# Kernel optimization log

Measured on AMD Instinct MI355X. Metric: run time of the kernel, lower is better.

The kernel has to match this reference:

```python
import jax, jax.numpy as jnp
import numpy as np

E = 768
H = 12
D = E // H  # 64


def setup_inputs() -> dict:
    key = jax.random.key(0)
    ks = jax.random.split(key, 12)
    B, S = 4, 2048
    scale = 1.0 / np.sqrt(E)
    inp = {
        "q": jax.random.normal(ks[0], (B, S, E), jnp.float32),
        "k": jax.random.normal(ks[1], (B, S, E), jnp.float32),
        "v": jax.random.normal(ks[2], (B, S, E), jnp.float32),
        "mask": jax.random.randint(ks[3], (B, S), 0, 2, jnp.int32),
        "Wq": jax.random.normal(ks[4], (E, E), jnp.float32) * scale,
        "bq": jnp.zeros((E,), jnp.float32),
        "Wk": jax.random.normal(ks[5], (E, E), jnp.float32) * scale,
        "bk": jnp.zeros((E,), jnp.float32),
        "Wv": jax.random.normal(ks[6], (E, E), jnp.float32) * scale,
        "bv": jnp.zeros((E,), jnp.float32),
        "Wo": jax.random.normal(ks[7], (E, E), jnp.float32) * scale,
        "bo": jnp.zeros((E,), jnp.float32),
    }
    return inp


def reference(q, k, v, mask, Wq, bq, Wk, bk, Wv, bv, Wo, bo):
    B, Sq, _ = q.shape
    Sk = k.shape[1]
    # QKV projections, split into heads: [B, H, S, D]
    qh = (q @ Wq + bq).reshape(B, Sq, H, D).transpose(0, 2, 1, 3)
    kh = (k @ Wk + bk).reshape(B, Sk, H, D).transpose(0, 2, 1, 3)
    vh = (v @ Wv + bv).reshape(B, Sk, H, D).transpose(0, 2, 1, 3)
    scores = jnp.einsum("bhqd,bhkd->bhqk", qh, kh) / jnp.sqrt(jnp.float32(D))
    # enc=True padding-mask path: positions where mask==0 get -1e9 added
    bias = jnp.where(mask == 0, jnp.float32(-1e9), jnp.float32(0.0))  # [B, Sk]
    scores = scores + bias[:, None, None, :]
    weights = jax.nn.softmax(scores, axis=-1)
    # dropout is identity in eval mode
    ctx = jnp.einsum("bhqk,bhkd->bqhd", weights, vh).reshape(B, Sq, E)
    return ctx @ Wo + bo
```

## Files before the change

kernel.cpp:

```cpp
#include <hip/hip_runtime.h>
#include <hip/hip_bf16.h>
#include <stdint.h>


typedef __bf16 bf16x8 __attribute__((ext_vector_type(8)));
typedef __bf16 bf16x4 __attribute__((ext_vector_type(4)));
typedef float floatx4 __attribute__((ext_vector_type(4)));

#define MFMA_BF16(a, b, c) __builtin_amdgcn_mfma_f32_16x16x32_bf16(a, b, c, 0, 0, 0)


__device__ __forceinline__ void glds16(const __bf16* g, __bf16* l) {
  __builtin_amdgcn_global_load_lds(
      (const __attribute__((address_space(1))) unsigned int*)g,
      (__attribute__((address_space(3))) unsigned int*)l, 16, 0, 0);
}

__global__ __launch_bounds__(256) void prep_transpose(
    const float* __restrict__ W0, const float* __restrict__ W1,
    const float* __restrict__ W2, const float* __restrict__ W3,
    __bf16* __restrict__ T0, __bf16* __restrict__ T1,
    __bf16* __restrict__ T2, __bf16* __restrict__ T3) {
  const int z = blockIdx.z;
  const float* W = (z == 0) ? W0 : (z == 1) ? W1 : (z == 2) ? W2 : W3;
  __bf16* T = (z == 0) ? T0 : (z == 1) ? T1 : (z == 2) ? T2 : T3;
  __shared__ float t[32][33];
  const int tx = threadIdx.x & 31, ty = threadIdx.x >> 5;
  const int kb = blockIdx.x * 32, nb = blockIdx.y * 32;
#pragma unroll
  for (int j = 0; j < 4; ++j)
    t[ty + j * 8][tx] = W[(size_t)(kb + ty + j * 8) * 768 + nb + tx];
  __syncthreads();
#pragma unroll
  for (int j = 0; j < 4; ++j)
    T[(size_t)(nb + ty + j * 8) * 768 + kb + tx] = (__bf16)t[tx][ty + j * 8];
}

__global__ __launch_bounds__(256) void qkv_gemm(
    const __bf16* __restrict__ Wtq, const __bf16* __restrict__ Wtk,
    const __bf16* __restrict__ Wtv, const float* __restrict__ Xq,
    const float* __restrict__ Xk, const float* __restrict__ Xv,
    const float* __restrict__ bq, const float* __restrict__ bk,
    const float* __restrict__ bv, __bf16* __restrict__ Qh,
    __bf16* __restrict__ Kh, __bf16* __restrict__ Vt) {
  __shared__ __align__(16) __bf16 As[128 * 32];
  __shared__ __align__(16) __bf16 Bs[128 * 32];
  const int z = blockIdx.z;
  const __bf16* Aop = (z == 0) ? Wtq : (z == 1) ? Wtk : Wtv;
  const float* Bop = (z == 0) ? Xq : (z == 1) ? Xk : Xv;
  const float* bias = (z == 0) ? bq : (z == 1) ? bk : bv;
  __bf16* Dst = (z == 0) ? Qh : (z == 1) ? Kh : Vt;
  const int m0 = blockIdx.x * 128, n0 = blockIdx.y * 128;

  const int tid = threadIdx.x, lane = tid & 63, w = tid >> 6;
  const int quad = lane >> 4, l16 = lane & 15;
  const int wm = (w >> 1) * 64, wn = (w & 1) * 64;

  const int garow = w * 32 + (lane >> 2);
  const int gacol = (lane & 3) * 8;
  const __bf16* gA = Aop + (size_t)(m0 + garow) * 768 + gacol;
  __bf16* lA = As + w * 1024;
  const int brow = tid >> 3, bcol = (tid & 7) * 4;

  floatx4 acc[4][4] = {};

  for (int k0 = 0; k0 < 768; k0 += 32) {
    __syncthreads();
    glds16(gA, lA);
    glds16(gA + (size_t)16 * 768, lA + 512);
    gA += 32;
    float4 f[4];
#pragma unroll
    for (int j = 0; j < 4; ++j)
      f[j] = *(const float4*)&Bop[(size_t)(n0 + brow + 32 * j) * 768 + k0 + bcol];
#pragma unroll
    for (int j = 0; j < 4; ++j) {
      bf16x4 pv;
      pv[0] = (__bf16)f[j].x; pv[1] = (__bf16)f[j].y;
      pv[2] = (__bf16)f[j].z; pv[3] = (__bf16)f[j].w;
      *(bf16x4*)&Bs[(brow + 32 * j) * 32 + bcol] = pv;
    }
    __syncthreads();
    bf16x8 af[4], bfr[4];
#pragma unroll
    for (int t = 0; t < 4; ++t) {
      af[t] = *(const bf16x8*)&As[(wm + t * 16 + l16) * 32 + quad * 8];
      bfr[t] = *(const bf16x8*)&Bs[(wn + t * 16 + l16) * 32 + quad * 8];
    }
#pragma unroll
    for (int mt = 0; mt < 4; ++mt)
#pragma unroll
      for (int nt = 0; nt < 4; ++nt)
        acc[mt][nt] = MFMA_BF16(af[mt], bfr[nt], acc[mt][nt]);
  }

#pragma unroll
  for (int mt = 0; mt < 4; ++mt) {
    const int e = m0 + wm + mt * 16 + quad * 4;
    const float4 b4 = *(const float4*)&bias[e];
    const int h = e >> 6, d = e & 63;
#pragma unroll
    for (int nt = 0; nt < 4; ++nt) {
      const int s = n0 + wn + nt * 16 + l16;
      const int bb = s >> 11, sr = s & 2047;
      const float v0 = acc[mt][nt][0] + b4.x;
      const float v1 = acc[mt][nt][1] + b4.y;
      const float v2 = acc[mt][nt][2] + b4.z;
      const float v3 = acc[mt][nt][3] + b4.w;
      if (z < 2) {
        bf16x4 pv;
        pv[0] = (__bf16)v0; pv[1] = (__bf16)v1; pv[2] = (__bf16)v2; pv[3] = (__bf16)v3;
        *(bf16x4*)&Dst[((size_t)(bb * 12 + h) * 2048 + sr) * 64 + d] = pv;
      } else {
        const size_t base = ((size_t)(bb * 12 + h) * 64 + d) * 2048 + sr;
        Dst[base] = (__bf16)v0;
        Dst[base + 2048] = (__bf16)v1;
        Dst[base + 4096] = (__bf16)v2;
        Dst[base + 6144] = (__bf16)v3;
      }
    }
  }
}

__global__ __launch_bounds__(256) void out_gemm(const __bf16* __restrict__ Wto,
                                                const __bf16* __restrict__ Ctx,
                                                const float* __restrict__ bo,
                                                float* __restrict__ Out) {
  __shared__ __align__(16) __bf16 As[128 * 32];
  __shared__ __align__(16) __bf16 Bs[128 * 32];
  const int m0 = blockIdx.x * 128, n0 = blockIdx.y * 128;
  const int tid = threadIdx.x, lane = tid & 63, w = tid >> 6;
  const int quad = lane >> 4, l16 = lane & 15;
  const int wm = (w >> 1) * 64, wn = (w & 1) * 64;

  const int grow = w * 32 + (lane >> 2);
  const int gcol = (lane & 3) * 8;
  const __bf16* gA = Wto + (size_t)(m0 + grow) * 768 + gcol;
  const __bf16* gB = Ctx + (size_t)(n0 + grow) * 768 + gcol;
  __bf16* lA = As + w * 1024;
  __bf16* lB = Bs + w * 1024;

  floatx4 acc[4][4] = {};
  for (int k0 = 0; k0 < 768; k0 += 32) {
    __syncthreads();
    glds16(gA, lA);
    glds16(gA + (size_t)16 * 768, lA + 512);
    glds16(gB, lB);
    glds16(gB + (size_t)16 * 768, lB + 512);
    gA += 32;
    gB += 32;
    __syncthreads();
    bf16x8 af[4], bfr[4];
#pragma unroll
    for (int t = 0; t < 4; ++t) {
      af[t] = *(const bf16x8*)&As[(wm + t * 16 + l16) * 32 + quad * 8];
      bfr[t] = *(const bf16x8*)&Bs[(wn + t * 16 + l16) * 32 + quad * 8];
    }
#pragma unroll
    for (int mt = 0; mt < 4; ++mt)
#pragma unroll
      for (int nt = 0; nt < 4; ++nt)
        acc[mt][nt] = MFMA_BF16(af[mt], bfr[nt], acc[mt][nt]);
  }

#pragma unroll
  for (int mt = 0; mt < 4; ++mt) {
    const int e = m0 + wm + mt * 16 + quad * 4;
    const float4 b4 = *(const float4*)&bo[e];
#pragma unroll
    for (int nt = 0; nt < 4; ++nt) {
      const int s = n0 + wn + nt * 16 + l16;
      float4 r;
      r.x = acc[mt][nt][0] + b4.x;
      r.y = acc[mt][nt][1] + b4.y;
      r.z = acc[mt][nt][2] + b4.z;
      r.w = acc[mt][nt][3] + b4.w;
      *(float4*)&Out[(size_t)s * 768 + e] = r;
    }
  }
}

__global__ __launch_bounds__(256) void attn_kernel(
    const __bf16* __restrict__ Qh, const __bf16* __restrict__ Kh,
    const __bf16* __restrict__ Vt, const int* __restrict__ mask,
    __bf16* __restrict__ ctx) {
  const int bh = blockIdx.y, b = bh / 12, h = bh - b * 12;
  const int tid = threadIdx.x, lane = tid & 63, w = tid >> 6;
  const int quad = lane >> 4, l16 = lane & 15;
  const int q0 = blockIdx.x * 128 + w * 32;

  __shared__ float biasS[2048];
  __shared__ __align__(16) __bf16 Ks[64 * 64];
  __shared__ __align__(16) __bf16 Vs[64 * 64];
  __shared__ __align__(16) __bf16 Plds[4][32][72];

  for (int i = tid; i < 2048; i += 256)
    biasS[i] = mask[b * 2048 + i] ? 0.0f : -1e5f;
  __syncthreads();

  const __bf16* Qbase = Qh + (size_t)bh * 2048 * 64;
  const __bf16* Kbase = Kh + (size_t)bh * 2048 * 64;
  const __bf16* Vbase = Vt + (size_t)bh * 64 * 2048;

  bf16x8 bqf[2][2];
#pragma unroll
  for (int qt = 0; qt < 2; ++qt)
#pragma unroll
    for (int c = 0; c < 2; ++c)
      bqf[qt][c] =
          *(const bf16x8*)&Qbase[(size_t)(q0 + qt * 16 + l16) * 64 + c * 32 + quad * 8];

  const int srow = (lane >> 3);
  const int scol = (lane & 7) * 8;

  floatx4 o[4][2] = {};
  float rS[2] = {0.0f, 0.0f};
  const float SC = 0.18033688011112042f;

  for (int kt = 0; kt < 2048; kt += 64) {
    __syncthreads();
#pragma unroll
    for (int j = 0; j < 2; ++j) {
      const int c = w * 2 + j;
      const int row = c * 8 + srow;
      glds16(&Kbase[(size_t)(kt + row) * 64 + scol], Ks + c * 512);
      glds16(&Vbase[(size_t)row * 2048 + kt + scol], Vs + c * 512);
    }
    __syncthreads();

    floatx4 sc[4][2];
#pragma unroll
    for (int t = 0; t < 4; ++t) {
      bf16x8 ak0 = *(const bf16x8*)&Ks[(t * 16 + l16) * 64 + quad * 8];
      bf16x8 ak1 = *(const bf16x8*)&Ks[(t * 16 + l16) * 64 + 32 + quad * 8];
#pragma unroll
      for (int qt = 0; qt < 2; ++qt) {
        floatx4 zz = {};
        zz = MFMA_BF16(ak0, bqf[qt][0], zz);
        zz = MFMA_BF16(ak1, bqf[qt][1], zz);
        sc[t][qt] = zz;
      }
    }
#pragma unroll
    for (int t = 0; t < 4; ++t) {
      const float4 kb = *(const float4*)&biasS[kt + t * 16 + quad * 4];
#pragma unroll
      for (int qt = 0; qt < 2; ++qt) {
        floatx4 p;
        p[0] = exp2f(fmaf(sc[t][qt][0], SC, kb.x));
        p[1] = exp2f(fmaf(sc[t][qt][1], SC, kb.y));
        p[2] = exp2f(fmaf(sc[t][qt][2], SC, kb.z));
        p[3] = exp2f(fmaf(sc[t][qt][3], SC, kb.w));
        sc[t][qt] = p;
        rS[qt] += p[0] + p[1] + p[2] + p[3];
      }
    }
#pragma unroll
    for (int qt = 0; qt < 2; ++qt)
#pragma unroll
      for (int t = 0; t < 4; ++t) {
        bf16x4 pv;
        pv[0] = (__bf16)sc[t][qt][0];
        pv[1] = (__bf16)sc[t][qt][1];
        pv[2] = (__bf16)sc[t][qt][2];
        pv[3] = (__bf16)sc[t][qt][3];
        *(bf16x4*)&Plds[w][qt * 16 + l16][t * 16 + quad * 4] = pv;
      }
#pragma unroll
    for (int c = 0; c < 2; ++c) {
      bf16x8 bp[2];
#pragma unroll
      for (int qt = 0; qt < 2; ++qt)
        bp[qt] = *(const bf16x8*)&Plds[w][qt * 16 + l16][c * 32 + quad * 8];
#pragma unroll
      for (int dt = 0; dt < 4; ++dt) {
        bf16x8 av = *(const bf16x8*)&Vs[(dt * 16 + l16) * 64 + c * 32 + quad * 8];
#pragma unroll
        for (int qt = 0; qt < 2; ++qt) o[dt][qt] = MFMA_BF16(av, bp[qt], o[dt][qt]);
      }
    }
  }

  float inv[2];
#pragma unroll
  for (int qt = 0; qt < 2; ++qt) {
    float s = rS[qt];
    s += __shfl_xor(s, 16, 64);
    s += __shfl_xor(s, 32, 64);
    inv[qt] = 1.0f / s;
  }
#pragma unroll
  for (int dt = 0; dt < 4; ++dt)
#pragma unroll
    for (int qt = 0; qt < 2; ++qt) {
      const int q = q0 + qt * 16 + l16;
      const int d = h * 64 + dt * 16 + quad * 4;
      bf16x4 pv;
      pv[0] = (__bf16)(o[dt][qt][0] * inv[qt]);
      pv[1] = (__bf16)(o[dt][qt][1] * inv[qt]);
      pv[2] = (__bf16)(o[dt][qt][2] * inv[qt]);
      pv[3] = (__bf16)(o[dt][qt][3] * inv[qt]);
      *(bf16x4*)&ctx[(size_t)(b * 2048 + q) * 768 + d] = pv;
    }
}

extern "C" void kernel_launch(void* const* d_in, const int* in_sizes, int n_in,
                              void* d_out, int out_size, void* d_ws, size_t ws_size,
                              hipStream_t stream) {
  const float* q = (const float*)d_in[0];
  const float* k = (const float*)d_in[1];
  const float* v = (const float*)d_in[2];
  const int* mask = (const int*)d_in[3];
  const float* Wq = (const float*)d_in[4];
  const float* bq = (const float*)d_in[5];
  const float* Wk = (const float*)d_in[6];
  const float* bk = (const float*)d_in[7];
  const float* Wv = (const float*)d_in[8];
  const float* bv = (const float*)d_in[9];
  const float* Wo = (const float*)d_in[10];
  const float* bo = (const float*)d_in[11];
  float* out = (float*)d_out;

  char* ws = (char*)d_ws;
  const size_t SZ = (size_t)8192 * 768 * 2;
  const size_t WSZ = (size_t)768 * 768 * 2;
  __bf16* Qh = (__bf16*)(ws);
  __bf16* Kh = (__bf16*)(ws + SZ);
  __bf16* Vt = (__bf16*)(ws + 2 * SZ);
  __bf16* ctx = (__bf16*)(ws + 3 * SZ);
  __bf16* Wtq = (__bf16*)(ws + 4 * SZ);
  __bf16* Wtk = (__bf16*)(ws + 4 * SZ + WSZ);
  __bf16* Wtv = (__bf16*)(ws + 4 * SZ + 2 * WSZ);
  __bf16* Wto = (__bf16*)(ws + 4 * SZ + 3 * WSZ);

  prep_transpose<<<dim3(24, 24, 4), 256, 0, stream>>>(Wq, Wk, Wv, Wo, Wtq, Wtk, Wtv, Wto);
  qkv_gemm<<<dim3(6, 64, 3), 256, 0, stream>>>(Wtq, Wtk, Wtv, q, k, v, bq, bk, bv,
                                               Qh, Kh, Vt);
  attn_kernel<<<dim3(16, 48), 256, 0, stream>>>(Qh, Kh, Vt, mask, ctx);
  out_gemm<<<dim3(6, 64), 256, 0, stream>>>(Wto, ctx, bo, out);
}
```

Baseline: 333.9 us.

## Pre-convert activations to bf16 and XOR-swizzle K/V layouts to avoid LDS conflicts

New measurement: 320.2 us. 4.1% less time.

```diff
diff --git a/kernel.cpp b/kernel.cpp
--- a/kernel.cpp
+++ b/kernel.cpp
@@ -14,6 +14,22 @@
   __builtin_amdgcn_global_load_lds(
       (const __attribute__((address_space(1))) unsigned int*)g,
       (__attribute__((address_space(3))) unsigned int*)l, 16, 0, 0);
+}
+
+__global__ __launch_bounds__(256) void prep_convert(
+    const float* __restrict__ q, const float* __restrict__ k,
+    const float* __restrict__ v, __bf16* __restrict__ Xq,
+    __bf16* __restrict__ Xk, __bf16* __restrict__ Xv) {
+  const int z = blockIdx.y;
+  const float* src = (z == 0) ? q : (z == 1) ? k : v;
+  __bf16* dst = (z == 0) ? Xq : (z == 1) ? Xk : Xv;
+  const size_t i8 = ((size_t)blockIdx.x * 256 + threadIdx.x) * 8;
+  float4 f0 = *(const float4*)&src[i8];
+  float4 f1 = *(const float4*)&src[i8 + 4];
+  bf16x8 o;
+  o[0] = (__bf16)f0.x; o[1] = (__bf16)f0.y; o[2] = (__bf16)f0.z; o[3] = (__bf16)f0.w;
+  o[4] = (__bf16)f1.x; o[5] = (__bf16)f1.y; o[6] = (__bf16)f1.z; o[7] = (__bf16)f1.w;
+  *(bf16x8*)&dst[i8] = o;
 }
 
 __global__ __launch_bounds__(256) void prep_transpose(
@@ -38,8 +54,8 @@
 
 __global__ __launch_bounds__(256) void qkv_gemm(
     const __bf16* __restrict__ Wtq, const __bf16* __restrict__ Wtk,
-    const __bf16* __restrict__ Wtv, const float* __restrict__ Xq,
-    const float* __restrict__ Xk, const float* __restrict__ Xv,
+    const __bf16* __restrict__ Wtv, const __bf16* __restrict__ Xq,
+    const __bf16* __restrict__ Xk, const __bf16* __restrict__ Xv,
     const float* __restrict__ bq, const float* __restrict__ bk,
     const float* __restrict__ bv, __bf16* __restrict__ Qh,
     __bf16* __restrict__ Kh, __bf16* __restrict__ Vt) {
@@ -47,7 +63,7 @@
   __shared__ __align__(16) __bf16 Bs[128 * 32];
   const int z = blockIdx.z;
   const __bf16* Aop = (z == 0) ? Wtq : (z == 1) ? Wtk : Wtv;
-  const float* Bop = (z == 0) ? Xq : (z == 1) ? Xk : Xv;
+  const __bf16* Bop = (z == 0) ? Xq : (z == 1) ? Xk : Xv;
   const float* bias = (z == 0) ? bq : (z == 1) ? bk : bv;
   __bf16* Dst = (z == 0) ? Qh : (z == 1) ? Kh : Vt;
   const int m0 = blockIdx.x * 128, n0 = blockIdx.y * 128;
@@ -56,11 +72,12 @@
   const int quad = lane >> 4, l16 = lane & 15;
   const int wm = (w >> 1) * 64, wn = (w & 1) * 64;
 
-  const int garow = w * 32 + (lane >> 2);
-  const int gacol = (lane & 3) * 8;
-  const __bf16* gA = Aop + (size_t)(m0 + garow) * 768 + gacol;
+  const int grow = w * 32 + (lane >> 2);
+  const int gcol = (lane & 3) * 8;
+  const __bf16* gA = Aop + (size_t)(m0 + grow) * 768 + gcol;
+  const __bf16* gB = Bop + (size_t)(n0 + grow) * 768 + gcol;
   __bf16* lA = As + w * 1024;
-  const int brow = tid >> 3, bcol = (tid & 7) * 4;
+  __bf16* lB = Bs + w * 1024;
 
   floatx4 acc[4][4] = {};
 
@@ -68,18 +85,10 @@
     __syncthreads();
     glds16(gA, lA);
     glds16(gA + (size_t)16 * 768, lA + 512);
+    glds16(gB, lB);
+    glds16(gB + (size_t)16 * 768, lB + 512);
     gA += 32;
-    float4 f[4];
-#pragma unroll
-    for (int j = 0; j < 4; ++j)
-      f[j] = *(const float4*)&Bop[(size_t)(n0 + brow + 32 * j) * 768 + k0 + bcol];
-#pragma unroll
-    for (int j = 0; j < 4; ++j) {
-      bf16x4 pv;
-      pv[0] = (__bf16)f[j].x; pv[1] = (__bf16)f[j].y;
-      pv[2] = (__bf16)f[j].z; pv[3] = (__bf16)f[j].w;
-      *(bf16x4*)&Bs[(brow + 32 * j) * 32 + bcol] = pv;
-    }
+    gB += 32;
     __syncthreads();
     bf16x8 af[4], bfr[4];
 #pragma unroll
@@ -110,13 +119,15 @@
       if (z < 2) {
         bf16x4 pv;
         pv[0] = (__bf16)v0; pv[1] = (__bf16)v1; pv[2] = (__bf16)v2; pv[3] = (__bf16)v3;
-        *(bf16x4*)&Dst[((size_t)(bb * 12 + h) * 2048 + sr) * 64 + d] = pv;
+        const int col = (z == 0) ? d : ((((d >> 3) ^ (sr & 7)) << 3) | (d & 7));
+        *(bf16x4*)&Dst[((size_t)(bb * 12 + h) * 2048 + sr) * 64 + col] = pv;
       } else {
-        const size_t base = ((size_t)(bb * 12 + h) * 64 + d) * 2048 + sr;
-        Dst[base] = (__bf16)v0;
-        Dst[base + 2048] = (__bf16)v1;
-        Dst[base + 4096] = (__bf16)v2;
-        Dst[base + 6144] = (__bf16)v3;
+        const size_t rowbase = ((size_t)(bb * 12 + h) * 64 + d) * 2048;
+        const int shi = sr & ~63, sblk = (sr >> 3) & 7, soff = sr & 7;
+        Dst[rowbase + 0 * 2048 + shi + (((sblk ^ ((d + 0) & 7))) << 3) + soff] = (__bf16)v0;
+        Dst[rowbase + 1 * 2048 + shi + (((sblk ^ ((d + 1) & 7))) << 3) + soff] = (__bf16)v1;
+        Dst[rowbase + 2 * 2048 + shi + (((sblk ^ ((d + 2) & 7))) << 3) + soff] = (__bf16)v2;
+        Dst[rowbase + 3 * 2048 + shi + (((sblk ^ ((d + 3) & 7))) << 3) + soff] = (__bf16)v3;
       }
     }
   }
@@ -212,6 +223,7 @@
 
   const int srow = (lane >> 3);
   const int scol = (lane & 7) * 8;
+  const int col0 = (quad ^ (l16 & 7)) * 8;
 
   floatx4 o[4][2] = {};
   float rS[2] = {0.0f, 0.0f};
@@ -231,8 +243,8 @@
     floatx4 sc[4][2];
 #pragma unroll
     for (int t = 0; t < 4; ++t) {
-      bf16x8 ak0 = *(const bf16x8*)&Ks[(t * 16 + l16) * 64 + quad * 8];
-      bf16x8 ak1 = *(const bf16x8*)&Ks[(t * 16 + l16) * 64 + 32 + quad * 8];
+      bf16x8 ak0 = *(const bf16x8*)&Ks[(t * 16 + l16) * 64 + col0];
+      bf16x8 ak1 = *(const bf16x8*)&Ks[(t * 16 + l16) * 64 + (col0 ^ 32)];
 #pragma unroll
       for (int qt = 0; qt < 2; ++qt) {
         floatx4 zz = {};
@@ -274,7 +286,7 @@
         bp[qt] = *(const bf16x8*)&Plds[w][qt * 16 + l16][c * 32 + quad * 8];
 #pragma unroll
       for (int dt = 0; dt < 4; ++dt) {
-        bf16x8 av = *(const bf16x8*)&Vs[(dt * 16 + l16) * 64 + c * 32 + quad * 8];
+        bf16x8 av = *(const bf16x8*)&Vs[(dt * 16 + l16) * 64 + (col0 ^ (c * 32))];
 #pragma unroll
         for (int qt = 0; qt < 2; ++qt) o[dt][qt] = MFMA_BF16(av, bp[qt], o[dt][qt]);
       }
@@ -324,17 +336,21 @@
   char* ws = (char*)d_ws;
   const size_t SZ = (size_t)8192 * 768 * 2;
   const size_t WSZ = (size_t)768 * 768 * 2;
-  __bf16* Qh = (__bf16*)(ws);
-  __bf16* Kh = (__bf16*)(ws + SZ);
-  __bf16* Vt = (__bf16*)(ws + 2 * SZ);
-  __bf16* ctx = (__bf16*)(ws + 3 * SZ);
-  __bf16* Wtq = (__bf16*)(ws + 4 * SZ);
-  __bf16* Wtk = (__bf16*)(ws + 4 * SZ + WSZ);
-  __bf16* Wtv = (__bf16*)(ws + 4 * SZ + 2 * WSZ);
-  __bf16* Wto = (__bf16*)(ws + 4 * SZ + 3 * WSZ);
-
+  __bf16* Xq = (__bf16*)(ws);
+  __bf16* Xk = (__bf16*)(ws + SZ);
+  __bf16* Xv = (__bf16*)(ws + 2 * SZ);
+  __bf16* Qh = (__bf16*)(ws + 3 * SZ);
+  __bf16* Kh = (__bf16*)(ws + 4 * SZ);
+  __bf16* Vt = (__bf16*)(ws + 5 * SZ);
+  __bf16* ctx = (__bf16*)(ws + 6 * SZ);
+  __bf16* Wtq = (__bf16*)(ws + 7 * SZ);
+  __bf16* Wtk = (__bf16*)(ws + 7 * SZ + WSZ);
+  __bf16* Wtv = (__bf16*)(ws + 7 * SZ + 2 * WSZ);
+  __bf16* Wto = (__bf16*)(ws + 7 * SZ + 3 * WSZ);
+
+  prep_convert<<<dim3(3072, 3), 256, 0, stream>>>(q, k, v, Xq, Xk, Xv);
   prep_transpose<<<dim3(24, 24, 4), 256, 0, stream>>>(Wq, Wk, Wv, Wo, Wtq, Wtk, Wtv, Wto);
-  qkv_gemm<<<dim3(6, 64, 3), 256, 0, stream>>>(Wtq, Wtk, Wtv, q, k, v, bq, bk, bv,
+  qkv_gemm<<<dim3(6, 64, 3), 256, 0, stream>>>(Wtq, Wtk, Wtv, Xq, Xk, Xv, bq, bk, bv,
                                                Qh, Kh, Vt);
   attn_kernel<<<dim3(16, 48), 256, 0, stream>>>(Qh, Kh, Vt, mask, ctx);
   out_gemm<<<dim3(6, 64), 256, 0, stream>>>(Wto, ctx, bo, out);
```

## Double-buffer K/V tiles, pre-swizzle K/V layout, read mask directly in attention

Applied to the files above, without the earlier changes.

Result: faster. 309.3 us (-7.3%).

```diff
diff --git a/kernel.cpp b/kernel.cpp
--- a/kernel.cpp
+++ b/kernel.cpp
@@ -110,13 +110,15 @@
       if (z < 2) {
         bf16x4 pv;
         pv[0] = (__bf16)v0; pv[1] = (__bf16)v1; pv[2] = (__bf16)v2; pv[3] = (__bf16)v3;
-        *(bf16x4*)&Dst[((size_t)(bb * 12 + h) * 2048 + sr) * 64 + d] = pv;
+        const int col = (z == 0) ? d : ((((d >> 3) ^ (sr & 7)) << 3) | (d & 7));
+        *(bf16x4*)&Dst[((size_t)(bb * 12 + h) * 2048 + sr) * 64 + col] = pv;
       } else {
-        const size_t base = ((size_t)(bb * 12 + h) * 64 + d) * 2048 + sr;
-        Dst[base] = (__bf16)v0;
-        Dst[base + 2048] = (__bf16)v1;
-        Dst[base + 4096] = (__bf16)v2;
-        Dst[base + 6144] = (__bf16)v3;
+        const size_t rowbase = ((size_t)(bb * 12 + h) * 64 + d) * 2048;
+        const int shi = sr & ~63, sblk = (sr >> 3) & 7, soff = sr & 7;
+        Dst[rowbase + 0 * 2048 + shi + (((sblk ^ ((d + 0) & 7))) << 3) + soff] = (__bf16)v0;
+        Dst[rowbase + 1 * 2048 + shi + (((sblk ^ ((d + 1) & 7))) << 3) + soff] = (__bf16)v1;
+        Dst[rowbase + 2 * 2048 + shi + (((sblk ^ ((d + 2) & 7))) << 3) + soff] = (__bf16)v2;
+        Dst[rowbase + 3 * 2048 + shi + (((sblk ^ ((d + 3) & 7))) << 3) + soff] = (__bf16)v3;
       }
     }
   }
@@ -189,18 +191,14 @@
   const int quad = lane >> 4, l16 = lane & 15;
   const int q0 = blockIdx.x * 128 + w * 32;
 
-  __shared__ float biasS[2048];
-  __shared__ __align__(16) __bf16 Ks[64 * 64];
-  __shared__ __align__(16) __bf16 Vs[64 * 64];
+  __shared__ __align__(16) __bf16 Ks[2][64 * 64];
+  __shared__ __align__(16) __bf16 Vs[2][64 * 64];
   __shared__ __align__(16) __bf16 Plds[4][32][72];
-
-  for (int i = tid; i < 2048; i += 256)
-    biasS[i] = mask[b * 2048 + i] ? 0.0f : -1e5f;
-  __syncthreads();
 
   const __bf16* Qbase = Qh + (size_t)bh * 2048 * 64;
   const __bf16* Kbase = Kh + (size_t)bh * 2048 * 64;
   const __bf16* Vbase = Vt + (size_t)bh * 64 * 2048;
+  const int* maskB = mask + b * 2048;
 
   bf16x8 bqf[2][2];
 #pragma unroll
@@ -210,29 +208,44 @@
       bqf[qt][c] =
           *(const bf16x8*)&Qbase[(size_t)(q0 + qt * 16 + l16) * 64 + c * 32 + quad * 8];
 
-  const int srow = (lane >> 3);
+  const int r0 = (w * 2) * 8 + (lane >> 3);
+  const int r1 = (w * 2 + 1) * 8 + (lane >> 3);
   const int scol = (lane & 7) * 8;
+  const int d0 = (w * 2) * 512;
+  const int d1 = (w * 2 + 1) * 512;
+  const int col0 = (quad ^ (l16 & 7)) * 8;
+
+  glds16(&Kbase[(size_t)r0 * 64 + scol], &Ks[0][d0]);
+  glds16(&Kbase[(size_t)r1 * 64 + scol], &Ks[0][d1]);
+  glds16(&Vbase[(size_t)r0 * 2048 + scol], &Vs[0][d0]);
+  glds16(&Vbase[(size_t)r1 * 2048 + scol], &Vs[0][d1]);
 
   floatx4 o[4][2] = {};
   float rS[2] = {0.0f, 0.0f};
   const float SC = 0.18033688011112042f;
 
-  for (int kt = 0; kt < 2048; kt += 64) {
-    __syncthreads();
-#pragma unroll
-    for (int j = 0; j < 2; ++j) {
-      const int c = w * 2 + j;
-      const int row = c * 8 + srow;
-      glds16(&Kbase[(size_t)(kt + row) * 64 + scol], Ks + c * 512);
-      glds16(&Vbase[(size_t)row * 2048 + kt + scol], Vs + c * 512);
-    }
-    __syncthreads();
+  for (int it = 0; it < 32; ++it) {
+    const int kt = it * 64;
+    const int cur = it & 1;
+    const int nxt = cur ^ 1;
+    const int nkt = (kt + 64) & 2047;
+
+    __syncthreads();
+
+    glds16(&Kbase[(size_t)(nkt + r0) * 64 + scol], &Ks[nxt][d0]);
+    glds16(&Kbase[(size_t)(nkt + r1) * 64 + scol], &Ks[nxt][d1]);
+    glds16(&Vbase[(size_t)r0 * 2048 + nkt + scol], &Vs[nxt][d0]);
+    glds16(&Vbase[(size_t)r1 * 2048 + nkt + scol], &Vs[nxt][d1]);
+
+    int4 mk[4];
+#pragma unroll
+    for (int t = 0; t < 4; ++t) mk[t] = *(const int4*)&maskB[kt + t * 16 + quad * 4];
 
     floatx4 sc[4][2];
 #pragma unroll
     for (int t = 0; t < 4; ++t) {
-      bf16x8 ak0 = *(const bf16x8*)&Ks[(t * 16 + l16) * 64 + quad * 8];
-      bf16x8 ak1 = *(const bf16x8*)&Ks[(t * 16 + l16) * 64 + 32 + quad * 8];
+      bf16x8 ak0 = *(const bf16x8*)&Ks[cur][(t * 16 + l16) * 64 + col0];
+      bf16x8 ak1 = *(const bf16x8*)&Ks[cur][(t * 16 + l16) * 64 + (col0 ^ 32)];
 #pragma unroll
       for (int qt = 0; qt < 2; ++qt) {
         floatx4 zz = {};
@@ -243,14 +256,17 @@
     }
 #pragma unroll
     for (int t = 0; t < 4; ++t) {
-      const float4 kb = *(const float4*)&biasS[kt + t * 16 + quad * 4];
+      const float k0f = mk[t].x ? 0.0f : -1e5f;
+      const float k1f = mk[t].y ? 0.0f : -1e5f;
+      const float k2f = mk[t].z ? 0.0f : -1e5f;
+      const float k3f = mk[t].w ? 0.0f : -1e5f;
 #pragma unroll
       for (int qt = 0; qt < 2; ++qt) {
         floatx4 p;
-        p[0] = exp2f(fmaf(sc[t][qt][0], SC, kb.x));
-        p[1] = exp2f(fmaf(sc[t][qt][1], SC, kb.y));
-        p[2] = exp2f(fmaf(sc[t][qt][2], SC, kb.z));
-        p[3] = exp2f(fmaf(sc[t][qt][3], SC, kb.w));
+        p[0] = __builtin_amdgcn_exp2f(fmaf(sc[t][qt][0], SC, k0f));
+        p[1] = __builtin_amdgcn_exp2f(fmaf(sc[t][qt][1], SC, k1f));
+        p[2] = __builtin_amdgcn_exp2f(fmaf(sc[t][qt][2], SC, k2f));
+        p[3] = __builtin_amdgcn_exp2f(fmaf(sc[t][qt][3], SC, k3f));
         sc[t][qt] = p;
         rS[qt] += p[0] + p[1] + p[2] + p[3];
       }
@@ -274,7 +290,7 @@
         bp[qt] = *(const bf16x8*)&Plds[w][qt * 16 + l16][c * 32 + quad * 8];
 #pragma unroll
       for (int dt = 0; dt < 4; ++dt) {
-        bf16x8 av = *(const bf16x8*)&Vs[(dt * 16 + l16) * 64 + c * 32 + quad * 8];
+        bf16x8 av = *(const bf16x8*)&Vs[cur][(dt * 16 + l16) * 64 + (col0 ^ (c * 32))];
 #pragma unroll
         for (int qt = 0; qt < 2; ++qt) o[dt][qt] = MFMA_BF16(av, bp[qt], o[dt][qt]);
       }
```
